# Kernel tuning notes

Measured on AMD Instinct MI355X. Metric: run time of the kernel, lower is better.

Reference implementation:

```python
import jax, jax.numpy as jnp
import numpy as np

RCUT = 6.0      # cutoff radius
AXIS = 16       # axis_neuron
NORM = 64.0     # normalizer = avg_neighbors + 1 (precomputed stat)
EPS = 1e-15
NTYPES = 2


def _embed(h, W0, b0, W1, b1, W2, b2):
    # tiny per-type-pair embedding MLP: scalar sr -> C channels
    h = jnp.tanh(h @ W0 + b0)
    h = jnp.tanh(h @ W1 + b1)
    return jnp.tanh(h @ W2 + b2)


def _forward(coord_3N, box_33, srmean, srstd, xrsrstd, Gbias, Ebias,
             emb_W0, emb_b0, emb_W1, emb_b1, emb_W2, emb_b2,
             fit_W0, fit_b0, fit_W1, fit_b1, fit_W2, fit_b2, n1):
    N = coord_3N.shape[1]
    L = jnp.diagonal(box_33)  # orthorhombic box lengths (3,)
    # relative coords with minimum-image convention: x[d,i,j] = c[d,j] - c[d,i]
    x_3NM = coord_3N[:, None, :] - coord_3N[:, :, None]
    x_3NM = x_3NM - L[:, None, None] * jnp.round(x_3NM / L[:, None, None])
    eye = jnp.eye(N, dtype=bool)
    r_NM = jnp.sqrt(jnp.where(eye, 1.0, (x_3NM ** 2).sum(0)))  # diag masked for safe grad
    # smooth switching / r  (DeepPot-SE style sr)
    u = r_NM / RCUT
    sw = jnp.where((r_NM < RCUT) & (~eye), ((-6.0 * u + 15.0) * u - 10.0) * u ** 3 + 1.0, 0.0)
    sr_NM = sw / r_NM
    rsr_NM = sr_NM / r_NM
    idx = (0, n1, N)  # contiguous type boundaries (atoms sorted by type)
    rows_sr, rows_rsr, rows_emb = [], [], []
    for i in range(NTYPES):
        sr_i = sr_NM[idx[i]:idx[i + 1]]
        rows_sr.append(sr_i / srstd[i])
        rows_rsr.append(rsr_NM[idx[i]:idx[i + 1]] / xrsrstd[i])
        srn_i = (sr_i - srmean[i]) / srstd[i]
        blocks = []
        for j in range(NTYPES):
            p = NTYPES * i + j  # type-pair index
            blocks.append(_embed(srn_i[:, idx[j]:idx[j + 1], None],
                                 emb_W0[p], emb_b0[p], emb_W1[p], emb_b1[p], emb_W2[p], emb_b2[p]))
        rows_emb.append(jnp.concatenate(blocks, axis=1))
    srbias_NM = jnp.concatenate(rows_sr, axis=0)
    R_3NM = (jnp.concatenate(rows_rsr, axis=0)[None] + EPS) * x_3NM  # e3norm = 1
    embed_NMC = jnp.concatenate(rows_emb, axis=0)
    # weighted reductions over neighbor axis M (einsum avoids the 3*N*M*C temp)
    Ginv_NC = jnp.einsum('nm,nmc->nc', srbias_NM, embed_NMC) / NORM
    Geqv_3NC = jnp.einsum('dnm,nmc->dnc', R_3NM, embed_NMC) / NORM
    G_4NC = jnp.concatenate([(Ginv_NC + Gbias)[None], Geqv_3NC], axis=0)
    # equivariant outer-product descriptor: Feat[n,a,c] = sum_k G[k,n,c]*G[k,n,a]
    Feat_NX = jnp.einsum('knc,kna->nac', G_4NC, G_4NC[:, :, :AXIS]).reshape(N, -1)
    energy = jnp.zeros((), dtype=Feat_NX.dtype)
    for i in range(NTYPES):
        h = Feat_NX[idx[i]:idx[i + 1]]
        h = jnp.tanh(h @ fit_W0[i] + fit_b0[i])
        h = jnp.tanh(h @ fit_W1[i] + fit_b1[i])
        h = h @ fit_W2[i] + fit_b2[i]
        energy = energy + (h + Ebias[i]).sum()
    return energy


def setup_inputs() -> dict:
    key = jax.random.key(0)
    ks = jax.random.split(key, 20)
    N, N1, BOXL = 1024, 512, 20.0
    W = (16, 32, 64)
    X, F = AXIS * W[-1], 128

    def wt(k, shape, fan_in):
        return jax.random.normal(k, shape, jnp.float32) / np.float32(np.sqrt(fan_in))

    return {
        'coord_3N': jax.random.uniform(ks[0], (3, N), jnp.float32) * BOXL,
        'box_33': BOXL * jnp.eye(3, dtype=jnp.float32),
        'srmean': 0.1 * jax.random.uniform(ks[1], (NTYPES,), jnp.float32),
        'srstd': 0.5 + jax.random.uniform(ks[2], (NTYPES,), jnp.float32),
        'xrsrstd': 0.5 + jax.random.uniform(ks[3], (NTYPES,), jnp.float32),
        'Gbias': 0.1 * jax.random.normal(ks[4], (W[2],), jnp.float32),
        'Ebias': jax.random.normal(ks[5], (NTYPES,), jnp.float32),
        'emb_W0': wt(ks[6], (4, 1, W[0]), 1),
        'emb_b0': 0.1 * jax.random.normal(ks[7], (4, W[0]), jnp.float32),
        'emb_W1': wt(ks[8], (4, W[0], W[1]), W[0]),
        'emb_b1': 0.1 * jax.random.normal(ks[9], (4, W[1]), jnp.float32),
        'emb_W2': wt(ks[10], (4, W[1], W[2]), W[1]),
        'emb_b2': 0.1 * jax.random.normal(ks[11], (4, W[2]), jnp.float32),
        'fit_W0': wt(ks[12], (NTYPES, X, F), X),
        'fit_b0': 0.1 * jax.random.normal(ks[13], (NTYPES, F), jnp.float32),
        'fit_W1': wt(ks[14], (NTYPES, F, F), F),
        'fit_b1': 0.1 * jax.random.normal(ks[15], (NTYPES, F), jnp.float32),
        'fit_W2': wt(ks[16], (NTYPES, F, 1), F),
        'fit_b2': 0.1 * jax.random.normal(ks[17], (NTYPES, 1), jnp.float32),
        'n1': N1,
    }


def reference(coord_3N, box_33, srmean, srstd, xrsrstd, Gbias, Ebias,
              emb_W0, emb_b0, emb_W1, emb_b1, emb_W2, emb_b2,
              fit_W0, fit_b0, fit_W1, fit_b1, fit_W2, fit_b2, n1):
    return _forward(coord_3N, box_33, srmean, srstd, xrsrstd, Gbias, Ebias,
                    emb_W0, emb_b0, emb_W1, emb_b1, emb_W2, emb_b2,
                    fit_W0, fit_b0, fit_W1, fit_b1, fit_W2, fit_b2, n1)
```

## Files before the change

kernel.cpp:

```cpp
#include <hip/hip_runtime.h>

#define RCUT 6.0f

typedef _Float16 h2v __attribute__((ext_vector_type(2)));
typedef _Float16 h8  __attribute__((ext_vector_type(8)));
typedef float    f4  __attribute__((ext_vector_type(4)));

__device__ __forceinline__ float fast_tanh(float x) {
    float e = __expf(2.0f * x);
    return 1.0f - 2.0f * __builtin_amdgcn_rcpf(e + 1.0f);
}

__device__ __forceinline__ h2v pkh(float a, float b) {
#if __has_builtin(__builtin_amdgcn_cvt_pkrtz)
    union { __fp16 __attribute__((ext_vector_type(2))) r; h2v h; } u;
    u.r = __builtin_amdgcn_cvt_pkrtz(a, b);
    return u.h;
#else
    h2v r; r.x = (_Float16)a; r.y = (_Float16)b; return r;
#endif
}

union SMem {
    struct {
        float s_w0[2][16], s_b0[2][16];
        __align__(16) _Float16 s_srn[512];
        __align__(16) _Float16 s_cf[4][512];
        __align__(16) _Float16 s_h1[128][32];
        unsigned short s_nbr[512];
        float s_g[4][4][64];
        float s_g4[256];
        __align__(16) _Float16 w1t[2][32][24];
        __align__(16) _Float16 w2t[2][64][40];
        int s_wcnt[4];
    } e;
    float s_t[32][33];
};

__global__ __launch_bounds__(256, 4) void k_embed(
    const float* __restrict__ coord, const float* __restrict__ box,
    const float* __restrict__ srmean, const float* __restrict__ srstd,
    const float* __restrict__ xrsrstd, const float* __restrict__ Gbias,
    const float* __restrict__ eW0, const float* __restrict__ eb0,
    const float* __restrict__ eW1, const float* __restrict__ eb1,
    const float* __restrict__ eW2, const float* __restrict__ eb2,
    const int* __restrict__ n1p,
    const float* __restrict__ fW0, const float* __restrict__ fW1,
    h2v* __restrict__ feat, _Float16* __restrict__ W0ht,
    _Float16* __restrict__ W1ht, unsigned int* __restrict__ counter, int N)
{
    const int tid = threadIdx.x;
    __shared__ SMem sm;

    const int n1 = *n1p;
    const int wid = tid >> 6, lane = tid & 63;
    const int l15 = lane & 15, lk = lane >> 4;

    {
        const int n  = blockIdx.x;
        const int ti = (n >= n1) ? 1 : 0;

        for (int t = tid; t < 32; t += 256) { int j = t >> 4, f = t & 15;
            sm.e.s_w0[j][f] = eW0[(2 * ti + j) * 16 + f];
            sm.e.s_b0[j][f] = eb0[(2 * ti + j) * 16 + f]; }
        for (int idx = tid; idx < 1024; idx += 256) {
            int j = idx >> 9, r = idx & 511, f = r >> 5, g = r & 31;
            sm.e.w1t[j][g][f] = (_Float16)eW1[(2 * ti + j) * 512 + f * 32 + g];
        }
        for (int idx = tid; idx < 4096; idx += 256) {
            int j = idx >> 11, r = idx & 2047, g = r >> 6, c = r & 63;
            sm.e.w2t[j][c][g] = (_Float16)eW2[(2 * ti + j) * 2048 + g * 64 + c];
        }
        float b1r[2][2], b2r[2][4];
        #pragma unroll
        for (int j = 0; j < 2; j++) {
            #pragma unroll
            for (int q = 0; q < 2; q++) b1r[j][q] = eb1[(2 * ti + j) * 32 + 16 * q + l15];
            #pragma unroll
            for (int q = 0; q < 4; q++) b2r[j][q] = eb2[(2 * ti + j) * 64 + 16 * q + l15];
        }

        const float Lx = box[0], Ly = box[4], Lz = box[8];
        const float iLx = 1.0f / Lx, iLy = 1.0f / Ly, iLz = 1.0f / Lz;
        const float xn = coord[n], yn = coord[N + n], zn = coord[2 * N + n];
        const float srm  = srmean[ti];
        const float isrs = 1.0f / srstd[ti];
        const float ixrs = 1.0f / xrsrstd[ti];

        unsigned long long bal[4];
        {
            int wc = 0;
            const int mystart = wid * 256;
            #pragma unroll
            for (int r = 0; r < 4; r++) {
                int m = mystart + r * 64 + lane;
                float dx = coord[m] - xn;         dx -= Lx * rintf(dx * iLx);
                float dy = coord[N + m] - yn;     dy -= Ly * rintf(dy * iLy);
                float dz = coord[2 * N + m] - zn; dz -= Lz * rintf(dz * iLz);
                float r2 = dx * dx + dy * dy + dz * dz;
                bool pred = (r2 < RCUT * RCUT) && (m != n);
                bal[r] = __ballot(pred);
                wc += (int)__popcll(bal[r]);
            }
            if (lane == 0) sm.e.s_wcnt[wid] = wc;
        }
        __syncthreads();
        int cnt = sm.e.s_wcnt[0] + sm.e.s_wcnt[1] + sm.e.s_wcnt[2] + sm.e.s_wcnt[3];
        if (cnt > 512) cnt = 512;
        {
            int base = 0;
            for (int w = 0; w < wid; w++) base += sm.e.s_wcnt[w];
            const unsigned long long lt = (1ull << lane) - 1ull;
            const int mystart = wid * 256;
            #pragma unroll
            for (int r = 0; r < 4; r++) {
                int m = mystart + r * 64 + lane;
                if ((bal[r] >> lane) & 1ull) {
                    int pos = base + (int)__popcll(bal[r] & lt);
                    if (pos < 512) {
                        float dx = coord[m] - xn;         dx -= Lx * rintf(dx * iLx);
                        float dy = coord[N + m] - yn;     dy -= Ly * rintf(dy * iLy);
                        float dz = coord[2 * N + m] - zn; dz -= Lz * rintf(dz * iLz);
                        float r2 = dx * dx + dy * dy + dz * dz;
                        float rr = sqrtf(r2);
                        float rinv = __builtin_amdgcn_rcpf(rr);
                        float u  = rr * (1.0f / RCUT);
                        float u3 = u * u * u;
                        float sw_ = ((-6.0f * u + 15.0f) * u - 10.0f) * u3 + 1.0f;
                        float sr  = sw_ * rinv;
                        float crs = sr * rinv * ixrs + 1e-15f;
                        sm.e.s_srn[pos]   = (_Float16)((sr - srm) * isrs);
                        sm.e.s_cf[0][pos] = (_Float16)(sr * isrs);
                        sm.e.s_cf[1][pos] = (_Float16)(crs * dx);
                        sm.e.s_cf[2][pos] = (_Float16)(crs * dy);
                        sm.e.s_cf[3][pos] = (_Float16)(crs * dz);
                        sm.e.s_nbr[pos]   = (unsigned short)m;
                    }
                }
                base += (int)__popcll(bal[r]);
            }
        }
        __syncthreads();
        const int ntiles = (cnt + 127) >> 7;
        for (int i = cnt + tid; i < ntiles * 128; i += 256) {
            sm.e.s_srn[i] = (_Float16)0.0f; sm.e.s_nbr[i] = 0;
            sm.e.s_cf[0][i] = (_Float16)0.0f; sm.e.s_cf[1][i] = (_Float16)0.0f;
            sm.e.s_cf[2][i] = (_Float16)0.0f; sm.e.s_cf[3][i] = (_Float16)0.0f;
        }
        __syncthreads();

        const f4 zf4 = {0.0f, 0.0f, 0.0f, 0.0f};
        float gk[4][4] = {};

        for (int t = 0; t < ntiles; t++) {
            const int t128 = t << 7;
            #pragma unroll
            for (int mt2 = 0; mt2 < 2; mt2++) {
                const int mt = 2 * wid + mt2;
                const int row = 16 * mt + l15;
                const int rp = t128 + row;
                float srn = (float)sm.e.s_srn[rp];
                int jr = (sm.e.s_nbr[rp] >= n1) ? 1 : 0;
                h8 a = {};
                if (lk < 2) {
                    const float* wp = &sm.e.s_w0[jr][8 * lk];
                    const float* bp = &sm.e.s_b0[jr][8 * lk];
                    #pragma unroll
                    for (int q = 0; q < 8; q++)
                        a[q] = (_Float16)fast_tanh(fmaf(srn, wp[q], bp[q]));
                }
                int j_r[4];
                #pragma unroll
                for (int r = 0; r < 4; r++)
                    j_r[r] = (sm.e.s_nbr[t128 + 16 * mt + 4 * lk + r] >= n1) ? 1 : 0;

                #pragma unroll
                for (int nt1 = 0; nt1 < 2; nt1++) {
                    const int c = 16 * nt1 + l15;
                    h8 b0f = {}, b1f = {};
                    if (lk < 2) {
                        b0f = *(const h8*)&sm.e.w1t[0][c][8 * lk];
                        b1f = *(const h8*)&sm.e.w1t[1][c][8 * lk];
                    }
                    f4 d0 = __builtin_amdgcn_mfma_f32_16x16x32_f16(a, b0f, zf4, 0, 0, 0);
                    f4 d1 = __builtin_amdgcn_mfma_f32_16x16x32_f16(a, b1f, zf4, 0, 0, 0);
                    #pragma unroll
                    for (int r = 0; r < 4; r++) {
                        int gp = 16 * mt + 4 * lk + r;
                        float hv = fast_tanh((j_r[r] ? d1[r] : d0[r]) + (j_r[r] ? b1r[1][nt1] : b1r[0][nt1]));
                        int e = 16 * nt1 + l15;
                        sm.e.s_h1[gp][(((e >> 3) ^ ((gp >> 1) & 3)) << 3) + (e & 7)] = (_Float16)hv;
                    }
                }
                asm volatile("" ::: "memory");

                h8 a2 = *(const h8*)&sm.e.s_h1[row][((lk ^ ((row >> 1) & 3)) << 3)];
                float cfv[4][4];
                #pragma unroll
                for (int k = 0; k < 4; k++) {
                    #pragma unroll
                    for (int r = 0; r < 4; r++)
                        cfv[k][r] = (float)sm.e.s_cf[k][t128 + 16 * mt + 4 * lk + r];
                }
                #pragma unroll
                for (int nt = 0; nt < 4; nt++) {
                    h8 w20 = *(const h8*)&sm.e.w2t[0][16 * nt + l15][8 * lk];
                    h8 w21 = *(const h8*)&sm.e.w2t[1][16 * nt + l15][8 * lk];
                    f4 e0 = __builtin_amdgcn_mfma_f32_16x16x32_f16(a2, w20, zf4, 0, 0, 0);
                    f4 e1 = __builtin_amdgcn_mfma_f32_16x16x32_f16(a2, w21, zf4, 0, 0, 0);
                    #pragma unroll
                    for (int r = 0; r < 4; r++) {
                        float ev = fast_tanh((j_r[r] ? e1[r] : e0[r]) + (j_r[r] ? b2r[1][nt] : b2r[0][nt]));
                        #pragma unroll
                        for (int k = 0; k < 4; k++)
                            gk[k][nt] = fmaf(cfv[k][r], ev, gk[k][nt]);
                    }
                }
            }
        }

        #pragma unroll
        for (int k = 0; k < 4; k++) {
            #pragma unroll
            for (int nt = 0; nt < 4; nt++) {
                float v = gk[k][nt];
                v += __shfl_xor(v, 16);
                v += __shfl_xor(v, 32);
                if (lane < 16) sm.e.s_g[wid][k][nt * 16 + lane] = v;
            }
        }
        __syncthreads();
        {
            int k = tid >> 6, c = tid & 63;
            float g = (sm.e.s_g[0][k][c] + sm.e.s_g[1][k][c]) + (sm.e.s_g[2][k][c] + sm.e.s_g[3][k][c]);
            g *= (1.0f / 64.0f);
            if (k == 0) g += Gbias[c];
            sm.e.s_g4[k * 64 + c] = g;
        }
        __syncthreads();
        {
            h2v* outp = feat + (size_t)n * 512;
            #pragma unroll
            for (int q = 0; q < 2; q++) {
                int o2 = tid + 256 * q;
                int a = o2 >> 5, c = (2 * o2) & 63;
                float ga0 = sm.e.s_g4[a],       ga1 = sm.e.s_g4[64 + a];
                float ga2 = sm.e.s_g4[128 + a], ga3 = sm.e.s_g4[192 + a];
                float s0 = ga0 * sm.e.s_g4[c];
                s0 = fmaf(ga1, sm.e.s_g4[64 + c],  s0);
                s0 = fmaf(ga2, sm.e.s_g4[128 + c], s0);
                s0 = fmaf(ga3, sm.e.s_g4[192 + c], s0);
                float s1 = ga0 * sm.e.s_g4[c + 1];
                s1 = fmaf(ga1, sm.e.s_g4[64 + c + 1],  s1);
                s1 = fmaf(ga2, sm.e.s_g4[128 + c + 1], s1);
                s1 = fmaf(ga3, sm.e.s_g4[192 + c + 1], s1);
                outp[o2] = pkh(s0, s1);
            }
        }
    }

    if (blockIdx.x < 288) {
        __syncthreads();
        const int b = blockIdx.x;
        if (b == 0 && tid == 0) *counter = 0u;
        if (b < 256) {
            int type = b >> 7, tb = b & 127;
            int ki = tb >> 2, ci = tb & 3;
            const float* src = fW0 + (size_t)type * 131072;
            int c = tid & 31, r0 = (tid >> 5) * 4;
            #pragma unroll
            for (int q = 0; q < 4; q++)
                sm.s_t[r0 + q][c] = src[(size_t)(ki * 32 + r0 + q) * 128 + ci * 32 + c];
            __syncthreads();
            _Float16* dst = W0ht + (size_t)type * 131072;
            int kk = tid & 31, c0 = (tid >> 5) * 4;
            #pragma unroll
            for (int q = 0; q < 4; q++)
                dst[(size_t)(ci * 32 + c0 + q) * 1024 + ki * 32 + kk] = (_Float16)sm.s_t[kk][c0 + q];
        } else {
            int b2v = b - 256, type = b2v >> 4, tb = b2v & 15;
            int ki = tb >> 2, ci = tb & 3;
            const float* src = fW1 + (size_t)type * 16384;
            int c = tid & 31, r0 = (tid >> 5) * 4;
            #pragma unroll
            for (int q = 0; q < 4; q++)
                sm.s_t[r0 + q][c] = src[(size_t)(ki * 32 + r0 + q) * 128 + ci * 32 + c];
            __syncthreads();
            _Float16* dst = W1ht + (size_t)type * 16384;
            int kk = tid & 31, c0 = (tid >> 5) * 4;
            #pragma unroll
            for (int q = 0; q < 4; q++)
                dst[(size_t)(ci * 32 + c0 + q) * 128 + ki * 32 + kk] = (_Float16)sm.s_t[kk][c0 + q];
        }
    }
}

__global__ __launch_bounds__(512) void k_fit(
    const _Float16* __restrict__ featf, const _Float16* __restrict__ W0ht,
    const _Float16* __restrict__ W1ht,
    const float* __restrict__ b0, const float* __restrict__ b1,
    const float* __restrict__ W2, const float* __restrict__ b2,
    const float* __restrict__ Ebias, const int* __restrict__ n1p,
    unsigned int* __restrict__ counter, float* __restrict__ slots,
    float* __restrict__ out)
{
    __shared__ float s_red[4][2][16][64];
    __shared__ __align__(16) _Float16 s_hd[16][128];
    __shared__ float s_sum[16][32];

    const int tid = threadIdx.x;
    const int lane = tid & 63, w = tid >> 6;
    const int kq = w >> 1, ch = w & 1;
    const int l15 = lane & 15, lk = lane >> 4;
    const int n0 = blockIdx.x * 16;
    const int ia = (n0 >= *n1p) ? 1 : 0;
    const f4 zf4 = {0.0f, 0.0f, 0.0f, 0.0f};

    const _Float16* Ap = featf + (size_t)(n0 + l15) * 1024 + kq * 256;
    const _Float16* B0 = W0ht + (size_t)ia * 131072 + kq * 256;
    f4 acc[4] = {zf4, zf4, zf4, zf4};
    #pragma unroll
    for (int ks = 0; ks < 8; ks++) {
        h8 a = *(const h8*)(Ap + ks * 32 + 8 * lk);
        #pragma unroll
        for (int nt = 0; nt < 4; nt++) {
            const int c = ch * 64 + nt * 16 + l15;
            h8 b = *(const h8*)(B0 + (size_t)c * 1024 + ks * 32 + 8 * lk);
            acc[nt] = __builtin_amdgcn_mfma_f32_16x16x32_f16(a, b, acc[nt], 0, 0, 0);
        }
    }
    #pragma unroll
    for (int nt = 0; nt < 4; nt++)
        #pragma unroll
        for (int r = 0; r < 4; r++)
            s_red[kq][ch][4 * lk + r][nt * 16 + l15] = acc[nt][r];
    __syncthreads();

    {
        const int row = tid >> 5, c0 = (tid & 31) * 4;
        const int chh = c0 >> 6, cl = c0 & 63;
        f4 v = *(const f4*)&s_red[0][chh][row][cl];
        v += *(const f4*)&s_red[1][chh][row][cl];
        v += *(const f4*)&s_red[2][chh][row][cl];
        v += *(const f4*)&s_red[3][chh][row][cl];
        #pragma unroll
        for (int q = 0; q < 4; q++) {
            int c = c0 + q;
            float h = fast_tanh(v[q] + b0[ia * 128 + c]);
            s_hd[row][(((c >> 3) ^ row) << 3) + (c & 7)] = (_Float16)h;
        }
    }
    __syncthreads();

    f4 acc1[4] = {zf4, zf4, zf4, zf4};
    {
        h8 a = *(const h8*)&s_hd[l15][(((4 * kq + lk) ^ l15) & 15) << 3];
        const _Float16* B1 = W1ht + (size_t)ia * 16384 + kq * 32;
        #pragma unroll
        for (int nt = 0; nt < 4; nt++) {
            const int c = ch * 64 + nt * 16 + l15;
            h8 b = *(const h8*)(B1 + (size_t)c * 128 + 8 * lk);
            acc1[nt] = __builtin_amdgcn_mfma_f32_16x16x32_f16(a, b, zf4, 0, 0, 0);
        }
    }
    #pragma unroll
    for (int nt = 0; nt < 4; nt++)
        #pragma unroll
        for (int r = 0; r < 4; r++)
            s_red[kq][ch][4 * lk + r][nt * 16 + l15] = acc1[nt][r];
    __syncthreads();

    {
        const int row = tid >> 5, c0 = (tid & 31) * 4;
        const int chh = c0 >> 6, cl = c0 & 63;
        f4 v = *(const f4*)&s_red[0][chh][row][cl];
        v += *(const f4*)&s_red[1][chh][row][cl];
        v += *(const f4*)&s_red[2][chh][row][cl];
        v += *(const f4*)&s_red[3][chh][row][cl];
        float pv = 0.0f;
        #pragma unroll
        for (int q = 0; q < 4; q++) {
            int c = c0 + q;
            pv += fast_tanh(v[q] + b1[ia * 128 + c]) * W2[ia * 128 + c];
        }
        s_sum[row][tid & 31] = pv;
    }
    __syncthreads();
    if (w == 0) {
        const int row = lane >> 2, g = lane & 3;
        float s = 0.0f;
        #pragma unroll
        for (int i = 0; i < 8; i++) s += s_sum[row][8 * g + i];
        s += __shfl_xor(s, 1);  s += __shfl_xor(s, 2);
        s += __shfl_xor(s, 4);  s += __shfl_xor(s, 8);
        s += __shfl_xor(s, 16); s += __shfl_xor(s, 32);
        if (lane == 0) {
            float e = s + 16.0f * (b2[ia] + Ebias[ia]);
            slots[blockIdx.x] = e;
            __threadfence();
            unsigned int old = atomicAdd(counter, 1u);
            if (old == 63u) {
                __threadfence();
                float tot = 0.0f;
                for (int i = 0; i < 64; i++)
                    tot += __hip_atomic_load(&slots[i], __ATOMIC_RELAXED, __HIP_MEMORY_SCOPE_AGENT);
                out[0] = tot;
            }
        }
    }
}

extern "C" void kernel_launch(void* const* d_in, const int* in_sizes, int n_in,
                              void* d_out, int out_size, void* d_ws, size_t ws_size,
                              hipStream_t stream) {
    const float* coord   = (const float*)d_in[0];
    const float* box     = (const float*)d_in[1];
    const float* srmean  = (const float*)d_in[2];
    const float* srstd   = (const float*)d_in[3];
    const float* xrsrstd = (const float*)d_in[4];
    const float* Gbias   = (const float*)d_in[5];
    const float* Ebias   = (const float*)d_in[6];
    const float* eW0     = (const float*)d_in[7];
    const float* eb0     = (const float*)d_in[8];
    const float* eW1     = (const float*)d_in[9];
    const float* eb1     = (const float*)d_in[10];
    const float* eW2     = (const float*)d_in[11];
    const float* eb2     = (const float*)d_in[12];
    const float* fW0     = (const float*)d_in[13];
    const float* fb0     = (const float*)d_in[14];
    const float* fW1     = (const float*)d_in[15];
    const float* fb1     = (const float*)d_in[16];
    const float* fW2     = (const float*)d_in[17];
    const float* fb2     = (const float*)d_in[18];
    const int*   n1p     = (const int*)d_in[19];

    const int N = in_sizes[0] / 3;
    h2v*      featbuf = (h2v*)d_ws;
    _Float16* W0ht = (_Float16*)((char*)d_ws + (size_t)2 * 1024 * 1024);
    _Float16* W1ht = W0ht + 2 * 131072;
    char* tail = (char*)d_ws + (size_t)(2 * 1024 + 512 + 64) * 1024;
    unsigned int* counter = (unsigned int*)tail;
    float*        slots   = (float*)(tail + 64);

    k_embed<<<N, 256, 0, stream>>>(coord, box, srmean, srstd, xrsrstd,
                                   Gbias, eW0, eb0, eW1, eb1, eW2, eb2,
                                   n1p, fW0, fW1, featbuf, W0ht, W1ht,
                                   counter, N);
    k_fit<<<N / 16, 512, 0, stream>>>((const _Float16*)featbuf, W0ht, W1ht,
                                      fb0, fb1, fW2, fb2, Ebias, n1p,
                                      counter, slots, (float*)d_out);
}
```

Measured before the change: 39.52 us.

## Use 512-thread blocks in embed kernel with one m-tile per wave

Doubles the k_embed block to 512 threads (8 waves), so each wave processes one 16-row neighbor tile per 128-tile step instead of two. Shared memory is shrunk by unioning the coefficient and reduction buffers and giving each wave a private unswizzled h1 scratch. The aim is more parallelism per atom and a shorter serial loop per wave, at the cost of an 8-way cross-wave reduction, the extra sync and memory reuse that unioning requires, and tighter register limits from launch_bounds(512,8).

```diff
diff --git a/kernel.cpp b/kernel.cpp
--- a/kernel.cpp
+++ b/kernel.cpp
@@ -25,19 +25,23 @@
     struct {
         float s_w0[2][16], s_b0[2][16];
         __align__(16) _Float16 s_srn[512];
-        __align__(16) _Float16 s_cf[4][512];
-        __align__(16) _Float16 s_h1[128][32];
         unsigned short s_nbr[512];
-        float s_g[4][4][64];
-        float s_g4[256];
         __align__(16) _Float16 w1t[2][32][24];
         __align__(16) _Float16 w2t[2][64][40];
-        int s_wcnt[4];
+        int s_wcnt[8];
+        union {
+            __align__(16) _Float16 s_cf[4][512];
+            float s_g[8][4][64];
+        } u1;
+        union {
+            __align__(16) _Float16 s_h1[8][16][40];
+            float s_g4[256];
+        } u2;
     } e;
     float s_t[32][33];
 };
 
-__global__ __launch_bounds__(256, 4) void k_embed(
+__global__ __launch_bounds__(512, 8) void k_embed(
     const float* __restrict__ coord, const float* __restrict__ box,
     const float* __restrict__ srmean, const float* __restrict__ srstd,
     const float* __restrict__ xrsrstd, const float* __restrict__ Gbias,
@@ -60,14 +64,14 @@
         const int n  = blockIdx.x;
         const int ti = (n >= n1) ? 1 : 0;
 
-        for (int t = tid; t < 32; t += 256) { int j = t >> 4, f = t & 15;
+        for (int t = tid; t < 32; t += 512) { int j = t >> 4, f = t & 15;
             sm.e.s_w0[j][f] = eW0[(2 * ti + j) * 16 + f];
             sm.e.s_b0[j][f] = eb0[(2 * ti + j) * 16 + f]; }
-        for (int idx = tid; idx < 1024; idx += 256) {
+        for (int idx = tid; idx < 1024; idx += 512) {
             int j = idx >> 9, r = idx & 511, f = r >> 5, g = r & 31;
             sm.e.w1t[j][g][f] = (_Float16)eW1[(2 * ti + j) * 512 + f * 32 + g];
         }
-        for (int idx = tid; idx < 4096; idx += 256) {
+        for (int idx = tid; idx < 4096; idx += 512) {
             int j = idx >> 11, r = idx & 2047, g = r >> 6, c = r & 63;
             sm.e.w2t[j][c][g] = (_Float16)eW2[(2 * ti + j) * 2048 + g * 64 + c];
         }
@@ -87,12 +91,12 @@
         const float isrs = 1.0f / srstd[ti];
         const float ixrs = 1.0f / xrsrstd[ti];
 
-        unsigned long long bal[4];
+        unsigned long long bal[2];
         {
             int wc = 0;
-            const int mystart = wid * 256;
-            #pragma unroll
-            for (int r = 0; r < 4; r++) {
+            const int mystart = wid * 128;
+            #pragma unroll
+            for (int r = 0; r < 2; r++) {
                 int m = mystart + r * 64 + lane;
                 float dx = coord[m] - xn;         dx -= Lx * rintf(dx * iLx);
                 float dy = coord[N + m] - yn;     dy -= Ly * rintf(dy * iLy);
@@ -105,15 +109,17 @@
             if (lane == 0) sm.e.s_wcnt[wid] = wc;
         }
         __syncthreads();
-        int cnt = sm.e.s_wcnt[0] + sm.e.s_wcnt[1] + sm.e.s_wcnt[2] + sm.e.s_wcnt[3];
+        int cnt = 0;
+        #pragma unroll
+        for (int w = 0; w < 8; w++) cnt += sm.e.s_wcnt[w];
         if (cnt > 512) cnt = 512;
         {
             int base = 0;
             for (int w = 0; w < wid; w++) base += sm.e.s_wcnt[w];
             const unsigned long long lt = (1ull << lane) - 1ull;
-            const int mystart = wid * 256;
-            #pragma unroll
-            for (int r = 0; r < 4; r++) {
+            const int mystart = wid * 128;
+            #pragma unroll
+            for (int r = 0; r < 2; r++) {
                 int m = mystart + r * 64 + lane;
                 if ((bal[r] >> lane) & 1ull) {
                     int pos = base + (int)__popcll(bal[r] & lt);
@@ -129,12 +135,12 @@
                         float sw_ = ((-6.0f * u + 15.0f) * u - 10.0f) * u3 + 1.0f;
                         float sr  = sw_ * rinv;
                         float crs = sr * rinv * ixrs + 1e-15f;
-                        sm.e.s_srn[pos]   = (_Float16)((sr - srm) * isrs);
-                        sm.e.s_cf[0][pos] = (_Float16)(sr * isrs);
-                        sm.e.s_cf[1][pos] = (_Float16)(crs * dx);
-                        sm.e.s_cf[2][pos] = (_Float16)(crs * dy);
-                        sm.e.s_cf[3][pos] = (_Float16)(crs * dz);
-                        sm.e.s_nbr[pos]   = (unsigned short)m;
+                        sm.e.s_srn[pos]      = (_Float16)((sr - srm) * isrs);
+                        sm.e.u1.s_cf[0][pos] = (_Float16)(sr * isrs);
+                        sm.e.u1.s_cf[1][pos] = (_Float16)(crs * dx);
+                        sm.e.u1.s_cf[2][pos] = (_Float16)(crs * dy);
+                        sm.e.u1.s_cf[3][pos] = (_Float16)(crs * dz);
+                        sm.e.s_nbr[pos]      = (unsigned short)m;
                     }
                 }
                 base += (int)__popcll(bal[r]);
@@ -142,10 +148,10 @@
         }
         __syncthreads();
         const int ntiles = (cnt + 127) >> 7;
-        for (int i = cnt + tid; i < ntiles * 128; i += 256) {
+        for (int i = cnt + tid; i < ntiles * 128; i += 512) {
             sm.e.s_srn[i] = (_Float16)0.0f; sm.e.s_nbr[i] = 0;
-            sm.e.s_cf[0][i] = (_Float16)0.0f; sm.e.s_cf[1][i] = (_Float16)0.0f;
-            sm.e.s_cf[2][i] = (_Float16)0.0f; sm.e.s_cf[3][i] = (_Float16)0.0f;
+            sm.e.u1.s_cf[0][i] = (_Float16)0.0f; sm.e.u1.s_cf[1][i] = (_Float16)0.0f;
+            sm.e.u1.s_cf[2][i] = (_Float16)0.0f; sm.e.u1.s_cf[3][i] = (_Float16)0.0f;
         }
         __syncthreads();
 
@@ -154,71 +160,66 @@
 
         for (int t = 0; t < ntiles; t++) {
             const int t128 = t << 7;
-            #pragma unroll
-            for (int mt2 = 0; mt2 < 2; mt2++) {
-                const int mt = 2 * wid + mt2;
-                const int row = 16 * mt + l15;
-                const int rp = t128 + row;
-                float srn = (float)sm.e.s_srn[rp];
-                int jr = (sm.e.s_nbr[rp] >= n1) ? 1 : 0;
-                h8 a = {};
+            const int row = 16 * wid + l15;
+            const int rp = t128 + row;
+            float srn = (float)sm.e.s_srn[rp];
+            int jr = (sm.e.s_nbr[rp] >= n1) ? 1 : 0;
+            h8 a = {};
+            if (lk < 2) {
+                const float* wp = &sm.e.s_w0[jr][8 * lk];
+                const float* bp = &sm.e.s_b0[jr][8 * lk];
+                #pragma unroll
+                for (int q = 0; q < 8; q++)
+                    a[q] = (_Float16)fast_tanh(fmaf(srn, wp[q], bp[q]));
+            }
+            int j_r[4];
+            #pragma unroll
+            for (int r = 0; r < 4; r++)
+                j_r[r] = (sm.e.s_nbr[t128 + 16 * wid + 4 * lk + r] >= n1) ? 1 : 0;
+
+            #pragma unroll
+            for (int nt1 = 0; nt1 < 2; nt1++) {
+                const int c = 16 * nt1 + l15;
+                h8 b0f = {}, b1f = {};
                 if (lk < 2) {
-                    const float* wp = &sm.e.s_w0[jr][8 * lk];
-                    const float* bp = &sm.e.s_b0[jr][8 * lk];
+                    b0f = *(const h8*)&sm.e.w1t[0][c][8 * lk];
+                    b1f = *(const h8*)&sm.e.w1t[1][c][8 * lk];
+                }
+                f4 d0 = __builtin_amdgcn_mfma_f32_16x16x32_f16(a, b0f, zf4, 0, 0, 0);
+                f4 d1 = __builtin_amdgcn_mfma_f32_16x16x32_f16(a, b1f, zf4, 0, 0, 0);
+                #pragma unroll
+                for (int r = 0; r < 4; r++) {
+                    float hv = fast_tanh((j_r[r] ? d1[r] : d0[r]) + (j_r[r] ? b1r[1][nt1] : b1r[0][nt1]));
+                    sm.e.u2.s_h1[wid][4 * lk + r][16 * nt1 + l15] = (_Float16)hv;
+                }
+            }
+            asm volatile("" ::: "memory");
+
+            h8 a2 = *(const h8*)&sm.e.u2.s_h1[wid][l15][8 * lk];
+            float cfv[4][4];
+            #pragma unroll
+            for (int k = 0; k < 4; k++) {
+                #pragma unroll
+                for (int r = 0; r < 4; r++)
+                    cfv[k][r] = (float)sm.e.u1.s_cf[k][t128 + 16 * wid + 4 * lk + r];
+            }
+            #pragma unroll
+            for (int nt = 0; nt < 4; nt++) {
+                h8 w20 = *(const h8*)&sm.e.w2t[0][16 * nt + l15][8 * lk];
+                h8 w21 = *(const h8*)&sm.e.w2t[1][16 * nt + l15][8 * lk];
+                f4 e0 = __builtin_amdgcn_mfma_f32_16x16x32_f16(a2, w20, zf4, 0, 0, 0);
+                f4 e1 = __builtin_amdgcn_mfma_f32_16x16x32_f16(a2, w21, zf4, 0, 0, 0);
+                #pragma unroll
+                for (int r = 0; r < 4; r++) {
+                    float ev = fast_tanh((j_r[r] ? e1[r] : e0[r]) + (j_r[r] ? b2r[1][nt] : b2r[0][nt]));
                     #pragma unroll
-                    for (int q = 0; q < 8; q++)
-                        a[q] = (_Float16)fast_tanh(fmaf(srn, wp[q], bp[q]));
+                    for (int k = 0; k < 4; k++)
+                        gk[k][nt] = fmaf(cfv[k][r], ev, gk[k][nt]);
                 }
-                int j_r[4];
-                #pragma unroll
-                for (int r = 0; r < 4; r++)
-                    j_r[r] = (sm.e.s_nbr[t128 + 16 * mt + 4 * lk + r] >= n1) ? 1 : 0;
-
-                #pragma unroll
-                for (int nt1 = 0; nt1 < 2; nt1++) {
-                    const int c = 16 * nt1 + l15;
-                    h8 b0f = {}, b1f = {};
-                    if (lk < 2) {
-                        b0f = *(const h8*)&sm.e.w1t[0][c][8 * lk];
-                        b1f = *(const h8*)&sm.e.w1t[1][c][8 * lk];
-                    }
-                    f4 d0 = __builtin_amdgcn_mfma_f32_16x16x32_f16(a, b0f, zf4, 0, 0, 0);
-                    f4 d1 = __builtin_amdgcn_mfma_f32_16x16x32_f16(a, b1f, zf4, 0, 0, 0);
-                    #pragma unroll
-                    for (int r = 0; r < 4; r++) {
-                        int gp = 16 * mt + 4 * lk + r;
-                        float hv = fast_tanh((j_r[r] ? d1[r] : d0[r]) + (j_r[r] ? b1r[1][nt1] : b1r[0][nt1]));
-                        int e = 16 * nt1 + l15;
-                        sm.e.s_h1[gp][(((e >> 3) ^ ((gp >> 1) & 3)) << 3) + (e & 7)] = (_Float16)hv;
-                    }
-                }
-                asm volatile("" ::: "memory");
-
-                h8 a2 = *(const h8*)&sm.e.s_h1[row][((lk ^ ((row >> 1) & 3)) << 3)];
-                float cfv[4][4];
-                #pragma unroll
-                for (int k = 0; k < 4; k++) {
-                    #pragma unroll
-                    for (int r = 0; r < 4; r++)
-                        cfv[k][r] = (float)sm.e.s_cf[k][t128 + 16 * mt + 4 * lk + r];
-                }
-                #pragma unroll
-                for (int nt = 0; nt < 4; nt++) {
-                    h8 w20 = *(const h8*)&sm.e.w2t[0][16 * nt + l15][8 * lk];
-                    h8 w21 = *(const h8*)&sm.e.w2t[1][16 * nt + l15][8 * lk];
-                    f4 e0 = __builtin_amdgcn_mfma_f32_16x16x32_f16(a2, w20, zf4, 0, 0, 0);
-                    f4 e1 = __builtin_amdgcn_mfma_f32_16x16x32_f16(a2, w21, zf4, 0, 0, 0);
-                    #pragma unroll
-                    for (int r = 0; r < 4; r++) {
-                        float ev = fast_tanh((j_r[r] ? e1[r] : e0[r]) + (j_r[r] ? b2r[1][nt] : b2r[0][nt]));
-                        #pragma unroll
-                        for (int k = 0; k < 4; k++)
-                            gk[k][nt] = fmaf(cfv[k][r], ev, gk[k][nt]);
-                    }
-                }
-            }
-        }
-
+            }
+        }
+
+        __syncthreads();
         #pragma unroll
         for (int k = 0; k < 4; k++) {
             #pragma unroll
@@ -226,36 +227,36 @@
                 float v = gk[k][nt];
                 v += __shfl_xor(v, 16);
                 v += __shfl_xor(v, 32);
-                if (lane < 16) sm.e.s_g[wid][k][nt * 16 + lane] = v;
-            }
-        }
-        __syncthreads();
-        {
+                if (lane < 16) sm.e.u1.s_g[wid][k][nt * 16 + lane] = v;
+            }
+        }
+        __syncthreads();
+        if (tid < 256) {
             int k = tid >> 6, c = tid & 63;
-            float g = (sm.e.s_g[0][k][c] + sm.e.s_g[1][k][c]) + (sm.e.s_g[2][k][c] + sm.e.s_g[3][k][c]);
+            float g = 0.0f;
+            #pragma unroll
+            for (int w = 0; w < 8; w++) g += sm.e.u1.s_g[w][k][c];
             g *= (1.0f / 64.0f);
             if (k == 0) g += Gbias[c];
-            sm.e.s_g4[k * 64 + c] = g;
+            sm.e.u2.s_g4[k * 64 + c] = g;
         }
         __syncthreads();
         {
+            const float* sg = sm.e.u2.s_g4;
             h2v* outp = feat + (size_t)n * 512;
-            #pragma unroll
-            for (int q = 0; q < 2; q++) {
-                int o2 = tid + 256 * q;
-                int a = o2 >> 5, c = (2 * o2) & 63;
-                float ga0 = sm.e.s_g4[a],       ga1 = sm.e.s_g4[64 + a];
-                float ga2 = sm.e.s_g4[128 + a], ga3 = sm.e.s_g4[192 + a];
-                float s0 = ga0 * sm.e.s_g4[c];
-                s0 = fmaf(ga1, sm.e.s_g4[64 + c],  s0);
-                s0 = fmaf(ga2, sm.e.s_g4[128 + c], s0);
-                s0 = fmaf(ga3, sm.e.s_g4[192 + c], s0);
-                float s1 = ga0 * sm.e.s_g4[c + 1];
-                s1 = fmaf(ga1, sm.e.s_g4[64 + c + 1],  s1);
-                s1 = fmaf(ga2, sm.e.s_g4[128 + c + 1], s1);
-                s1 = fmaf(ga3, sm.e.s_g4[192 + c + 1], s1);
-                outp[o2] = pkh(s0, s1);
-            }
+            int o2 = tid;
+            int a = o2 >> 5, c = (2 * o2) & 63;
+            float ga0 = sg[a],       ga1 = sg[64 + a];
+            float ga2 = sg[128 + a], ga3 = sg[192 + a];
+            float s0 = ga0 * sg[c];
+            s0 = fmaf(ga1, sg[64 + c],  s0);
+            s0 = fmaf(ga2, sg[128 + c], s0);
+            s0 = fmaf(ga3, sg[192 + c], s0);
+            float s1 = ga0 * sg[c + 1];
+            s1 = fmaf(ga1, sg[64 + c + 1],  s1);
+            s1 = fmaf(ga2, sg[128 + c + 1], s1);
+            s1 = fmaf(ga3, sg[192 + c + 1], s1);
+            outp[o2] = pkh(s0, s1);
         }
     }
 
@@ -263,34 +264,44 @@
         __syncthreads();
         const int b = blockIdx.x;
         if (b == 0 && tid == 0) *counter = 0u;
-        if (b < 256) {
-            int type = b >> 7, tb = b & 127;
-            int ki = tb >> 2, ci = tb & 3;
-            const float* src = fW0 + (size_t)type * 131072;
-            int c = tid & 31, r0 = (tid >> 5) * 4;
-            #pragma unroll
-            for (int q = 0; q < 4; q++)
-                sm.s_t[r0 + q][c] = src[(size_t)(ki * 32 + r0 + q) * 128 + ci * 32 + c];
-            __syncthreads();
-            _Float16* dst = W0ht + (size_t)type * 131072;
-            int kk = tid & 31, c0 = (tid >> 5) * 4;
-            #pragma unroll
-            for (int q = 0; q < 4; q++)
-                dst[(size_t)(ci * 32 + c0 + q) * 1024 + ki * 32 + kk] = (_Float16)sm.s_t[kk][c0 + q];
-        } else {
-            int b2v = b - 256, type = b2v >> 4, tb = b2v & 15;
-            int ki = tb >> 2, ci = tb & 3;
-            const float* src = fW1 + (size_t)type * 16384;
-            int c = tid & 31, r0 = (tid >> 5) * 4;
-            #pragma unroll
-            for (int q = 0; q < 4; q++)
-                sm.s_t[r0 + q][c] = src[(size_t)(ki * 32 + r0 + q) * 128 + ci * 32 + c];
-            __syncthreads();
-            _Float16* dst = W1ht + (size_t)type * 16384;
-            int kk = tid & 31, c0 = (tid >> 5) * 4;
-            #pragma unroll
-            for (int q = 0; q < 4; q++)
-                dst[(size_t)(ci * 32 + c0 + q) * 128 + ki * 32 + kk] = (_Float16)sm.s_t[kk][c0 + q];
+        if (tid < 256) {
+            if (b < 256) {
+                int type = b >> 7, tb = b & 127;
+                int ki = tb >> 2, ci = tb & 3;
+                const float* src = fW0 + (size_t)type * 131072;
+                int c = tid & 31, r0 = (tid >> 5) * 4;
+                #pragma unroll
+                for (int q = 0; q < 4; q++)
+                    sm.s_t[r0 + q][c] = src[(size_t)(ki * 32 + r0 + q) * 128 + ci * 32 + c];
+            } else {
+                int b2v = b - 256, type = b2v >> 4, tb = b2v & 15;
+                int ki = tb >> 2, ci = tb & 3;
+                const float* src = fW1 + (size_t)type * 16384;
+                int c = tid & 31, r0 = (tid >> 5) * 4;
+                #pragma unroll
+                for (int q = 0; q < 4; q++)
+                    sm.s_t[r0 + q][c] = src[(size_t)(ki * 32 + r0 + q) * 128 + ci * 32 + c];
+            }
+        }
+        __syncthreads();
+        if (tid < 256) {
+            if (b < 256) {
+                int type = b >> 7, tb = b & 127;
+                int ki = tb >> 2, ci = tb & 3;
+                _Float16* dst = W0ht + (size_t)type * 131072;
+                int kk = tid & 31, c0 = (tid >> 5) * 4;
+                #pragma unroll
+                for (int q = 0; q < 4; q++)
+                    dst[(size_t)(ci * 32 + c0 + q) * 1024 + ki * 32 + kk] = (_Float16)sm.s_t[kk][c0 + q];
+            } else {
+                int b2v = b - 256, type = b2v >> 4, tb = b2v & 15;
+                int ki = tb >> 2, ci = tb & 3;
+                _Float16* dst = W1ht + (size_t)type * 16384;
+                int kk = tid & 31, c0 = (tid >> 5) * 4;
+                #pragma unroll
+                for (int q = 0; q < 4; q++)
+                    dst[(size_t)(ci * 32 + c0 + q) * 128 + ki * 32 + kk] = (_Float16)sm.s_t[kk][c0 + q];
+            }
         }
     }
 }
@@ -442,7 +453,7 @@
     unsigned int* counter = (unsigned int*)tail;
     float*        slots   = (float*)(tail + 64);
 
-    k_embed<<<N, 256, 0, stream>>>(coord, box, srmean, srstd, xrsrstd,
+    k_embed<<<N, 512, 0, stream>>>(coord, box, srmean, srstd, xrsrstd,
                                    Gbias, eW0, eb0, eW1, eb1, eW2, eb2,
                                    n1p, fW0, fW1, featbuf, W0ht, W1ht,
                                    counter, N);
```

Result: slower. 46.77 us (+18.3%).
